# Kernel tuning notes

Hardware: AMD Instinct MI355X
Metric: run time of the kernel (lower is better)

The kernel has to match this reference:

```python
import jax, jax.numpy as jnp
import numpy as np

WIDTH = 36
N = WIDTH * WIDTH          # 1296 graph nodes per patch
SIGMA = 0.01               # weight_sigma
ZMAX = 0.01                # support_zmax
U_MIN, U_MAX = 0.001, 1.0
N_ITERS = 9                # 1 initial qpsolve + 8 glr refinements


def _build_graph():
    # 4-connected grid graph on WIDTH x WIDTH pixels -> incidence matrix H [E, N]
    nodes = np.arange(N).reshape(WIDTH, WIDTH)
    i0 = np.concatenate([nodes[:, :-1].ravel(), nodes[:-1, :].ravel()])
    i1 = np.concatenate([nodes[:, 1:].ravel(), nodes[1:, :].ravel()])
    E = i0.shape[0]  # 2520
    H = np.zeros((E, N), np.float32)
    H[np.arange(E), i0] = 1.0
    H[np.arange(E), i1] = -1.0
    return i0.astype(np.int32), i1.astype(np.int32), H


def setup_inputs() -> dict:
    key = jax.random.key(0)
    ks = jax.random.split(key, 6)
    B = 2
    i0, i1, H = _build_graph()
    std = 0.02  # weights_init_normal
    return {
        "xf": jax.random.normal(ks[0], (B, 3, WIDTH, WIDTH), jnp.float32),
        "u_param": jax.random.uniform(ks[1], (1,), jnp.float32),
        "H": jnp.asarray(H),
        "cw_in": std * jax.random.normal(ks[2], (32, 3, 3, 3), jnp.float32),
        "b_in": jnp.zeros((32,), jnp.float32),
        "cw_mid": std * jax.random.normal(ks[3], (5, 32, 32, 3, 3), jnp.float32),
        "b_mid": jnp.zeros((5, 32), jnp.float32),
        "cw_out": std * jax.random.normal(ks[4], (6, 32, 3, 3), jnp.float32),
        "b_out": jnp.zeros((6,), jnp.float32),
        "idx0": jnp.asarray(i0),
        "idx1": jnp.asarray(i1),
    }


def _conv(x, w, b):
    y = jax.lax.conv_general_dilated(x, w, (1, 1), "SAME",
                                     dimension_numbers=("NCHW", "OIHW", "NCHW"))
    return y + b[None, :, None, None]


def _cnnf(x, cw_in, b_in, cw_mid, b_mid, cw_out, b_out):
    h = jax.nn.relu(_conv(x, cw_in, b_in))
    for i in range(cw_mid.shape[0]):
        h = jax.nn.relu(_conv(h, cw_mid[i], b_mid[i]))
    return _conv(h, cw_out, b_out)


def _forward(xf, u_param, H, cw_in, b_in, cw_mid, b_mid, cw_out, b_out, idx0, idx1):
    B, C = xf.shape[0], xf.shape[1]
    Ne = idx0.shape[0]
    u = jnp.clip(u_param, U_MIN, U_MAX)[0]  # cnnu == uu(): scalar u, clamped

    y = xf.reshape(B, C, N, 1)
    # edge weights from deep features: w = exp(-sum_f (H f)^2 / sigma^2)
    feat = _cnnf(xf, cw_in, b_in, cw_mid, b_mid, cw_out, b_out).reshape(B, 6, N, 1)
    Fs = jnp.einsum("en,bfno->bfeo", H, feat) ** 2          # [B,6,E,1]
    w = jnp.exp(-Fs.sum(axis=1) / (SIGMA ** 2))              # [B,E,1]
    wv = jnp.broadcast_to(w[:, None, :, 0], (B, C, Ne))      # repeat over channels

    eye = jnp.eye(N, dtype=xf.dtype)
    base = jnp.zeros((B, C, N, N), xf.dtype)                 # base_W

    def step(y):
        z = jnp.einsum("en,bcno->bceo", H, y)                # per-edge diffs [B,C,E,1]
        za = jnp.abs(z[..., 0])                              # [B,C,E]
        Wm = base.at[:, :, idx0, idx1].set(wv).at[:, :, idx1, idx0].set(wv)
        Zm = base.at[:, :, idx0, idx1].set(za).at[:, :, idx1, idx0].set(za)
        Zm = jnp.maximum(Zm, ZMAX)
        Lm = Wm / Zm                                         # reweighted adjacency
        deg = Lm.sum(axis=-1)                                # L @ ones(N,1)
        L = deg[..., :, None] * eye - Lm                     # graph Laplacian
        # qpsolve: GLR closed form  (I + u L) x = y
        return jnp.linalg.solve(eye + u * L, y)

    for _ in range(N_ITERS):
        y = step(y)
    return y.reshape(B, C, WIDTH, WIDTH)


def reference(xf, u_param, H, cw_in, b_in, cw_mid, b_mid, cw_out, b_out, idx0, idx1):
    return _forward(xf, u_param, H, cw_in, b_in, cw_mid, b_mid, cw_out, b_out, idx0, idx1)
```

## Files before the change

### kernel.cpp

```cpp
#include <hip/hip_runtime.h>
#include <math.h>

#define NN 1296
#define OFF 40
#define TOT (OFF + NN + 40)
#define KMAX 240
#define PXW 21

__global__ __launch_bounds__(256) void conv_in_k(
    const float* __restrict__ in, const float* __restrict__ wgt,
    const float* __restrict__ bias, float* __restrict__ out)
{
  const int gid = blockIdx.x * 256 + threadIdx.x;
  const int wid = gid >> 6, lane = gid & 63;
  if (wid >= 2 * 32 * PXW) return;
  const int px = (wid % PXW) * 64 + lane;
  const int co = __builtin_amdgcn_readfirstlane((wid / PXW) % 32);
  const int b  = __builtin_amdgcn_readfirstlane(wid / (PXW * 32));
  if (px >= NN) return;

  const int py = px / 36, pxx = px % 36;
  int offs[9]; float msk[9];
#pragma unroll
  for (int dy = 0; dy < 3; ++dy)
#pragma unroll
    for (int dx = 0; dx < 3; ++dx) {
      const int yy = py + dy - 1, xx = pxx + dx - 1;
      const bool okp = ((unsigned)yy < 36u) && ((unsigned)xx < 36u);
      offs[dy * 3 + dx] = okp ? (yy * 36 + xx) : 0;
      msk[dy * 3 + dx]  = okp ? 1.f : 0.f;
    }

  float acc = bias[co];
  const float* __restrict__ inp = in + (size_t)b * 3 * NN;
  const float* __restrict__ wB  = wgt + (size_t)co * 3 * 9;
#pragma unroll
  for (int ci = 0; ci < 3; ++ci) {
    float v[9];
#pragma unroll
    for (int k9 = 0; k9 < 9; ++k9) v[k9] = msk[k9] * inp[ci * NN + offs[k9]];
#pragma unroll
    for (int k9 = 0; k9 < 9; ++k9) acc = fmaf(v[k9], wB[ci * 9 + k9], acc);
  }
  out[(size_t)(b * 32 + co) * NN + px] = fmaxf(acc, 0.f);
}

__global__ __launch_bounds__(256) void conv_mid2_k(
    const float* __restrict__ in, const float* __restrict__ wgt,
    const float* __restrict__ bias, float* __restrict__ out)
{
  const int blk = blockIdx.x;
  const int pxg = blk % PXW;
  const int cog = (blk / PXW) & 3;
  const int b   = blk / (PXW * 4);
  const int lane = threadIdx.x & 63;
  const int ciq  = __builtin_amdgcn_readfirstlane(threadIdx.x >> 6);
  const int px   = pxg * 64 + lane;
  const bool ok  = px < NN;

  __shared__ float part[4][8][64];

  float acc[8] = {0.f, 0.f, 0.f, 0.f, 0.f, 0.f, 0.f, 0.f};
  if (ok) {
    const int py = px / 36, pxx = px % 36;
    int offs[9]; float msk[9];
#pragma unroll
    for (int dy = 0; dy < 3; ++dy)
#pragma unroll
      for (int dx = 0; dx < 3; ++dx) {
        const int yy = py + dy - 1, xx = pxx + dx - 1;
        const bool okp = ((unsigned)yy < 36u) && ((unsigned)xx < 36u);
        offs[dy * 3 + dx] = okp ? (yy * 36 + xx) : 0;
        msk[dy * 3 + dx]  = okp ? 1.f : 0.f;
      }
    const float* __restrict__ inp = in + ((size_t)b * 32 + ciq * 8) * NN;
    const float* __restrict__ wB = wgt + ((size_t)(cog * 8) * 32 + ciq * 8) * 9;
#pragma unroll
    for (int ci = 0; ci < 8; ++ci) {
      float v[9];
#pragma unroll
      for (int k9 = 0; k9 < 9; ++k9) v[k9] = msk[k9] * inp[ci * NN + offs[k9]];
#pragma unroll
      for (int t = 0; t < 8; ++t)
#pragma unroll
        for (int k9 = 0; k9 < 9; ++k9)
          acc[t] = fmaf(v[k9], wB[(t * 32 + ci) * 9 + k9], acc[t]);
    }
  }
#pragma unroll
  for (int t = 0; t < 8; ++t) part[ciq][t][lane] = acc[t];
  __syncthreads();
  if (ok) {
#pragma unroll
    for (int tt = 0; tt < 2; ++tt) {
      const int t = ciq + tt * 4;
      float s = part[0][t][lane] + part[1][t][lane]
              + part[2][t][lane] + part[3][t][lane] + bias[cog * 8 + t];
      s = fmaxf(s, 0.f);
      out[((size_t)b * 32 + cog * 8 + t) * NN + px] = s;
    }
  }
}

template<int COUT, bool RELU>
__global__ __launch_bounds__(256) void conv_mid_k(
    const float* __restrict__ in, const float* __restrict__ wgt,
    const float* __restrict__ bias, float* __restrict__ out)
{
  const int blk = blockIdx.x;
  const int pxg = blk % PXW;
  const int co  = (blk / PXW) % COUT;
  const int b   = blk / (PXW * COUT);
  const int lane = threadIdx.x & 63;
  const int ciq  = threadIdx.x >> 6;
  const int px   = pxg * 64 + lane;
  const bool ok  = px < NN;

  __shared__ float part[4][64];

  float acc = 0.f;
  if (ok) {
    const int py = px / 36, pxx = px % 36;
    int offs[9]; float msk[9];
#pragma unroll
    for (int dy = 0; dy < 3; ++dy)
#pragma unroll
      for (int dx = 0; dx < 3; ++dx) {
        const int yy = py + dy - 1, xx = pxx + dx - 1;
        const bool okp = ((unsigned)yy < 36u) && ((unsigned)xx < 36u);
        offs[dy * 3 + dx] = okp ? (yy * 36 + xx) : 0;
        msk[dy * 3 + dx]  = okp ? 1.f : 0.f;
      }
    const float* __restrict__ inp = in + ((size_t)b * 32 + ciq * 8) * NN;
    const float* __restrict__ wB  = wgt + ((size_t)co * 32 + ciq * 8) * 9;
#pragma unroll
    for (int ci = 0; ci < 8; ++ci) {
      float v[9];
#pragma unroll
      for (int k9 = 0; k9 < 9; ++k9) v[k9] = msk[k9] * inp[ci * NN + offs[k9]];
#pragma unroll
      for (int k9 = 0; k9 < 9; ++k9) acc = fmaf(v[k9], wB[ci * 9 + k9], acc);
    }
  }
  part[ciq][lane] = acc;
  __syncthreads();
  if (threadIdx.x < 64 && ok) {
    float s = part[0][lane] + part[1][lane] + part[2][lane] + part[3][lane]
            + bias[co];
    if (RELU) s = fmaxf(s, 0.f);
    out[((size_t)b * COUT + co) * NN + px] = s;
  }
}

__global__ __launch_bounds__(384) void gtv_k(
    const float* __restrict__ xf, const float* __restrict__ up,
    const float* __restrict__ feat, float* __restrict__ out)
{
  const int sys = blockIdx.x, b = sys / 3, ch = sys % 3;
  const int tid = threadIdx.x;
  const int wave = tid >> 6, lane = tid & 63;
  const bool act = tid < 324;
  const int qq = act ? tid : 0;
  const int i0 = OFF + 4 * qq;

  __shared__ __align__(16) float ysL[TOT], ahL[TOT], avL[TOT], dA[TOT], dB[TOT];
  __shared__ float red[16];

  float u = up[0]; u = fminf(fmaxf(u, 0.001f), 1.0f);

  if (tid < OFF) {
    const int t2 = OFF + NN + tid;
    ysL[tid] = 0.f; ahL[tid] = 0.f; avL[tid] = 0.f; dA[tid] = 0.f; dB[tid] = 0.f;
    ysL[t2] = 0.f; ahL[t2] = 0.f; avL[t2] = 0.f; dA[t2] = 0.f; dB[t2] = 0.f;
  }

  const float* __restrict__ xfB = xf + (size_t)(b * 3 + ch) * NN;
  float wh4[4] = {0.f, 0.f, 0.f, 0.f}, wv4[4] = {0.f, 0.f, 0.f, 0.f};
  if (act) {
    *(float4*)&ysL[i0] = *(const float4*)&xfB[4 * qq];
#pragma unroll
    for (int j = 0; j < 4; ++j) {
      const int n = 4 * qq + j;
      const int col = n % 36, row = n / 36;
      float sh = 0.f, sv = 0.f;
#pragma unroll
      for (int f = 0; f < 6; ++f) {
        const float* __restrict__ fp = feat + (size_t)(b * 6 + f) * NN;
        const float a = fp[n];
        if (col < 35) { const float d = a - fp[n + 1];  sh += d * d; }
        if (row < 35) { const float d = a - fp[n + 36]; sv += d * d; }
      }
      wh4[j] = (col < 35) ? expf(-sh * 1e4f) : 0.f;
      wv4[j] = (row < 35) ? expf(-sv * 1e4f) : 0.f;
    }
  }
  __syncthreads();

  float x[4] = {0.f, 0.f, 0.f, 0.f};

  for (int it = 0; it < 9; ++it) {
    float4 yv = make_float4(0,0,0,0), yD = make_float4(0,0,0,0);
    float yR = 0.f;
    float ah[4] = {0,0,0,0}, av[4] = {0,0,0,0};
    if (act) {
      yv = *(const float4*)&ysL[i0];
      yR = ysL[i0 + 4];
      yD = *(const float4*)&ysL[i0 + 36];
      ah[0] = u * wh4[0] / fmaxf(fabsf(yv.x - yv.y), 0.01f);
      ah[1] = u * wh4[1] / fmaxf(fabsf(yv.y - yv.z), 0.01f);
      ah[2] = u * wh4[2] / fmaxf(fabsf(yv.z - yv.w), 0.01f);
      ah[3] = u * wh4[3] / fmaxf(fabsf(yv.w - yR  ), 0.01f);
      av[0] = u * wv4[0] / fmaxf(fabsf(yv.x - yD.x), 0.01f);
      av[1] = u * wv4[1] / fmaxf(fabsf(yv.y - yD.y), 0.01f);
      av[2] = u * wv4[2] / fmaxf(fabsf(yv.z - yD.z), 0.01f);
      av[3] = u * wv4[3] / fmaxf(fabsf(yv.w - yD.w), 0.01f);
      *(float4*)&ahL[i0] = make_float4(ah[0], ah[1], ah[2], ah[3]);
      *(float4*)&avL[i0] = make_float4(av[0], av[1], av[2], av[3]);
    }
    __syncthreads();

    float cL[4], cR[4], cU[4], cD[4], cc[4], bn[4], os[4];
    float mo = 0.f, me = 0.f;
    if (act) {
      const float cl0 = ahL[i0 - 1];
      const float4 aU = *(const float4*)&avL[i0 - 36];
      cL[0] = cl0;  cL[1] = ah[0]; cL[2] = ah[1]; cL[3] = ah[2];
      cR[0] = ah[0]; cR[1] = ah[1]; cR[2] = ah[2]; cR[3] = ah[3];
      cU[0] = aU.x; cU[1] = aU.y; cU[2] = aU.z; cU[3] = aU.w;
      cD[0] = av[0]; cD[1] = av[1]; cD[2] = av[2]; cD[3] = av[3];
      bn[0] = yv.x; bn[1] = yv.y; bn[2] = yv.z; bn[3] = yv.w;
#pragma unroll
      for (int j = 0; j < 4; ++j) {
        os[j] = cL[j] + cR[j] + cU[j] + cD[j];
        cc[j] = 1.f + os[j];
        mo = fmaxf(mo, os[j]);
      }
      const float ahR  = ahL[i0 + 4];
      const float avRu = avL[i0 - 32];
      const float avR  = avL[i0 + 4];
      const float osR  = ah[3] + ahR + avRu + avR;
      const float ahDl = ahL[i0 + 35];
      const float4 ahD = *(const float4*)&ahL[i0 + 36];
      const float4 avD = *(const float4*)&avL[i0 + 36];
      float osD[4];
      osD[0] = ahDl  + ahD.x + av[0] + avD.x;
      osD[1] = ahD.x + ahD.y + av[1] + avD.y;
      osD[2] = ahD.y + ahD.z + av[2] + avD.z;
      osD[3] = ahD.z + ahD.w + av[3] + avD.w;
      const float osN[4] = { os[1], os[2], os[3], osR };
#pragma unroll
      for (int j = 0; j < 4; ++j)
        me = fmaxf(me, os[j] + fmaxf(osN[j], osD[j]));
    } else {
#pragma unroll
      for (int j = 0; j < 4; ++j) {
        cL[j]=cR[j]=cU[j]=cD[j]=0.f; cc[j]=1.f; bn[j]=0.f; os[j]=0.f;
      }
    }
#pragma unroll
    for (int o = 32; o >= 1; o >>= 1) {
      mo = fmaxf(mo, __shfl_xor(mo, o));
      me = fmaxf(me, __shfl_xor(me, o));
    }
    if (lane == 0) { red[wave] = mo; red[8 + wave] = me; }
    __syncthreads();
    float m1 = fmaxf(fmaxf(red[0], red[1]),
               fmaxf(fmaxf(red[2], red[3]), fmaxf(red[4], red[5])));
    float m2 = fmaxf(fmaxf(red[8], red[9]),
               fmaxf(fmaxf(red[10], red[11]), fmaxf(red[12], red[13])));
    const float lmaxL = fminf(2.f * m1, m2);

    const float h     = 0.5f * lmaxL;
    const float theta = 1.f + h;
    const float del   = fmaxf(h, 1e-30f);
    const float sig1  = theta / del;
    const float rho0  = del / theta;
    const float kappa = 1.f + lmaxL;
    const float srk   = sqrtf(kappa);
    const float rc    = (srk - 1.f) / (srk + 1.f);

    float r[4], d[4];
    float rmx = 0.f;
    if (act) {
      const float bl = ysL[i0 - 1];
      const float4 bu = *(const float4*)&ysL[i0 - 36];
      const float uu[4] = {bu.x, bu.y, bu.z, bu.w};
      const float dd[4] = {yD.x, yD.y, yD.z, yD.w};
#pragma unroll
      for (int j = 0; j < 4; ++j) {
        const float nl = (j == 0) ? bl : bn[j - 1];
        const float nr = (j == 3) ? yR : bn[j + 1];
        const float Ab = cc[j] * bn[j] - cL[j] * nl - cR[j] * nr
                       - cU[j] * uu[j] - cD[j] * dd[j];
        x[j] = bn[j];
        r[j] = bn[j] - Ab;
        d[j] = r[j] / theta;
        rmx = fmaxf(rmx, fabsf(r[j]));
      }
      *(float4*)&dB[i0] = make_float4(d[0], d[1], d[2], d[3]);
    } else {
#pragma unroll
      for (int j = 0; j < 4; ++j) { r[j] = 0.f; d[j] = 0.f; x[j] = 0.f; }
    }
#pragma unroll
    for (int o = 32; o >= 1; o >>= 1) rmx = fmaxf(rmx, __shfl_xor(rmx, o));
    if (lane == 0) red[wave] = rmx;
    __syncthreads();
    const float rmax0 = fmaxf(fmaxf(red[0], red[1]),
                       fmaxf(fmaxf(red[2], red[3]), fmaxf(red[4], red[5])));

    int kcap;
    if (rmax0 <= 5e-4f) kcap = 0;
    else if (rc < 1e-10f) kcap = 1;
    else {
      kcap = (int)ceilf(8.0f / (-logf(rc)));
      kcap = (kcap < 1) ? 1 : (kcap > KMAX ? KMAX : kcap);
    }
    const float eps = fmaxf(rmax0 * 3.3e-4f, 2.5e-4f);

    float rho = rho0;
    float* dc = dB; float* dnx = dA;
    for (int k = 0; k < kcap; ++k) {
      if (k >= 4 && (k & 3) == 0) {
        const float rmc = fmaxf(fmaxf(red[0], red[1]),
                         fmaxf(fmaxf(red[2], red[3]), fmaxf(red[4], red[5])));
        if (rmc <= eps) break;
      }
      const float rn = 1.f / (2.f * sig1 - rho);
      const float cd = rn * rho, cr = 2.f * rn / del;
      rho = rn;
      if (act) {
        const float dl = dc[i0 - 1], dr = dc[i0 + 4];
        const float4 u4 = *(const float4*)&dc[i0 - 36];
        const float4 d4 = *(const float4*)&dc[i0 + 36];
        const float uu[4] = {u4.x, u4.y, u4.z, u4.w};
        const float dd[4] = {d4.x, d4.y, d4.z, d4.w};
        float dn[4];
#pragma unroll
        for (int j = 0; j < 4; ++j) {
          const float nl = (j == 0) ? dl : d[j - 1];
          const float nr = (j == 3) ? dr : d[j + 1];
          const float Ad = cc[j] * d[j] - cL[j] * nl - cR[j] * nr
                         - cU[j] * uu[j] - cD[j] * dd[j];
          x[j] += d[j];
          r[j] -= Ad;
          dn[j] = cd * d[j] + cr * r[j];
        }
        *(float4*)&dnx[i0] = make_float4(dn[0], dn[1], dn[2], dn[3]);
#pragma unroll
        for (int j = 0; j < 4; ++j) d[j] = dn[j];
      }
      if ((k & 3) == 3) {
        float rm = 0.f;
        if (act) {
          rm = fmaxf(fmaxf(fabsf(r[0]), fabsf(r[1])),
                     fmaxf(fabsf(r[2]), fabsf(r[3])));
        }
#pragma unroll
        for (int o = 32; o >= 1; o >>= 1) rm = fmaxf(rm, __shfl_xor(rm, o));
        if (lane == 0) red[wave] = rm;
      }
      __syncthreads();
      float* t = dc; dc = dnx; dnx = t;
    }

    if (act) *(float4*)&ysL[i0] = make_float4(x[0], x[1], x[2], x[3]);
    __syncthreads();
  }

  if (act) *(float4*)&out[(size_t)(b * 3 + ch) * NN + 4 * qq]
      = make_float4(x[0], x[1], x[2], x[3]);
}

extern "C" void kernel_launch(void* const* d_in, const int* in_sizes, int n_in,
                              void* d_out, int out_size, void* d_ws, size_t ws_size,
                              hipStream_t stream) {
  const float* xf     = (const float*)d_in[0];
  const float* up     = (const float*)d_in[1];
  const float* cw_in  = (const float*)d_in[3];
  const float* b_in   = (const float*)d_in[4];
  const float* cw_mid = (const float*)d_in[5];
  const float* b_mid  = (const float*)d_in[6];
  const float* cw_out = (const float*)d_in[7];
  const float* b_out  = (const float*)d_in[8];

  float* ws   = (float*)d_ws;
  float* hb0  = ws;
  float* hb1  = hb0 + 82944;
  float* feat = hb1 + 82944;

  conv_in_k<<<dim3(336), dim3(256), 0, stream>>>(xf, cw_in, b_in, hb0);
  const float* src = hb0; float* dst = hb1;
  for (int i = 0; i < 5; ++i) {
    conv_mid2_k<<<dim3(2 * 4 * PXW), dim3(256), 0, stream>>>(
        src, cw_mid + i * 9216, b_mid + i * 32, dst);
    const float* t = dst; dst = (float*)src; src = t;
  }
  conv_mid_k<6, false><<<dim3(2 * 6 * PXW), dim3(256), 0, stream>>>(
      src, cw_out, b_out, feat);

  gtv_k<<<dim3(6), dim3(384), 0, stream>>>(xf, up, feat, (float*)d_out);
}
```

Measured before the change: 121.9 us.

## Fuse output conv into GTV solver and drop early-exit residual checks

The final 32->6 convolution is folded into the GTV solver kernel, so each block computes the feature maps into shared memory rather than launching a separate kernel and going through global memory. The periodic residual max-reduction and early-break test inside the Chebyshev-style iteration loop are removed, and the iteration-count heuristic constant drops from 8 to 7. This removes one launch and the per-4-iteration reduction overhead. In exchange, only 6 blocks now compute the output conv redundantly (each recomputes all 6 features per batch), and the loop always runs its full capped count, which may cost accuracy or extra iterations.

```diff
diff --git a/kernel.cpp b/kernel.cpp
--- a/kernel.cpp
+++ b/kernel.cpp
@@ -102,59 +102,10 @@
   }
 }
 
-template<int COUT, bool RELU>
-__global__ __launch_bounds__(256) void conv_mid_k(
-    const float* __restrict__ in, const float* __restrict__ wgt,
-    const float* __restrict__ bias, float* __restrict__ out)
-{
-  const int blk = blockIdx.x;
-  const int pxg = blk % PXW;
-  const int co  = (blk / PXW) % COUT;
-  const int b   = blk / (PXW * COUT);
-  const int lane = threadIdx.x & 63;
-  const int ciq  = threadIdx.x >> 6;
-  const int px   = pxg * 64 + lane;
-  const bool ok  = px < NN;
-
-  __shared__ float part[4][64];
-
-  float acc = 0.f;
-  if (ok) {
-    const int py = px / 36, pxx = px % 36;
-    int offs[9]; float msk[9];
-#pragma unroll
-    for (int dy = 0; dy < 3; ++dy)
-#pragma unroll
-      for (int dx = 0; dx < 3; ++dx) {
-        const int yy = py + dy - 1, xx = pxx + dx - 1;
-        const bool okp = ((unsigned)yy < 36u) && ((unsigned)xx < 36u);
-        offs[dy * 3 + dx] = okp ? (yy * 36 + xx) : 0;
-        msk[dy * 3 + dx]  = okp ? 1.f : 0.f;
-      }
-    const float* __restrict__ inp = in + ((size_t)b * 32 + ciq * 8) * NN;
-    const float* __restrict__ wB  = wgt + ((size_t)co * 32 + ciq * 8) * 9;
-#pragma unroll
-    for (int ci = 0; ci < 8; ++ci) {
-      float v[9];
-#pragma unroll
-      for (int k9 = 0; k9 < 9; ++k9) v[k9] = msk[k9] * inp[ci * NN + offs[k9]];
-#pragma unroll
-      for (int k9 = 0; k9 < 9; ++k9) acc = fmaf(v[k9], wB[ci * 9 + k9], acc);
-    }
-  }
-  part[ciq][lane] = acc;
-  __syncthreads();
-  if (threadIdx.x < 64 && ok) {
-    float s = part[0][lane] + part[1][lane] + part[2][lane] + part[3][lane]
-            + bias[co];
-    if (RELU) s = fmaxf(s, 0.f);
-    out[((size_t)b * COUT + co) * NN + px] = s;
-  }
-}
-
 __global__ __launch_bounds__(384) void gtv_k(
     const float* __restrict__ xf, const float* __restrict__ up,
-    const float* __restrict__ feat, float* __restrict__ out)
+    const float* __restrict__ mid, const float* __restrict__ cw_out,
+    const float* __restrict__ b_out, float* __restrict__ out)
 {
   const int sys = blockIdx.x, b = sys / 3, ch = sys % 3;
   const int tid = threadIdx.x;
@@ -164,6 +115,7 @@
   const int i0 = OFF + 4 * qq;
 
   __shared__ __align__(16) float ysL[TOT], ahL[TOT], avL[TOT], dA[TOT], dB[TOT];
+  __shared__ float featL[6 * NN];
   __shared__ float red[16];
 
   float u = up[0]; u = fminf(fmaxf(u, 0.001f), 1.0f);
@@ -175,9 +127,45 @@
   }
 
   const float* __restrict__ xfB = xf + (size_t)(b * 3 + ch) * NN;
+  if (act) {
+    *(float4*)&ysL[i0] = *(const float4*)&xfB[4 * qq];
+    const float* __restrict__ mB = mid + (size_t)b * 32 * NN;
+#pragma unroll
+    for (int j = 0; j < 4; ++j) {
+      const int n = 4 * qq + j;
+      const int py = n / 36, pxx = n % 36;
+      int offs[9]; float msk[9];
+#pragma unroll
+      for (int dy = 0; dy < 3; ++dy)
+#pragma unroll
+        for (int dx = 0; dx < 3; ++dx) {
+          const int yy = py + dy - 1, xx = pxx + dx - 1;
+          const bool okp = ((unsigned)yy < 36u) && ((unsigned)xx < 36u);
+          offs[dy * 3 + dx] = okp ? (yy * 36 + xx) : 0;
+          msk[dy * 3 + dx]  = okp ? 1.f : 0.f;
+        }
+      float accf[6];
+#pragma unroll
+      for (int f = 0; f < 6; ++f) accf[f] = b_out[f];
+#pragma unroll
+      for (int ci = 0; ci < 32; ++ci) {
+        float v[9];
+#pragma unroll
+        for (int k9 = 0; k9 < 9; ++k9) v[k9] = msk[k9] * mB[ci * NN + offs[k9]];
+#pragma unroll
+        for (int f = 0; f < 6; ++f)
+#pragma unroll
+          for (int k9 = 0; k9 < 9; ++k9)
+            accf[f] = fmaf(v[k9], cw_out[(f * 32 + ci) * 9 + k9], accf[f]);
+      }
+#pragma unroll
+      for (int f = 0; f < 6; ++f) featL[f * NN + n] = accf[f];
+    }
+  }
+  __syncthreads();
+
   float wh4[4] = {0.f, 0.f, 0.f, 0.f}, wv4[4] = {0.f, 0.f, 0.f, 0.f};
   if (act) {
-    *(float4*)&ysL[i0] = *(const float4*)&xfB[4 * qq];
 #pragma unroll
     for (int j = 0; j < 4; ++j) {
       const int n = 4 * qq + j;
@@ -185,7 +173,7 @@
       float sh = 0.f, sv = 0.f;
 #pragma unroll
       for (int f = 0; f < 6; ++f) {
-        const float* __restrict__ fp = feat + (size_t)(b * 6 + f) * NN;
+        const float* __restrict__ fp = featL + f * NN;
         const float a = fp[n];
         if (col < 35) { const float d = a - fp[n + 1];  sh += d * d; }
         if (row < 35) { const float d = a - fp[n + 36]; sv += d * d; }
@@ -313,19 +301,13 @@
     if (rmax0 <= 5e-4f) kcap = 0;
     else if (rc < 1e-10f) kcap = 1;
     else {
-      kcap = (int)ceilf(8.0f / (-logf(rc)));
+      kcap = (int)ceilf(7.0f / (-logf(rc)));
       kcap = (kcap < 1) ? 1 : (kcap > KMAX ? KMAX : kcap);
     }
-    const float eps = fmaxf(rmax0 * 3.3e-4f, 2.5e-4f);
 
     float rho = rho0;
     float* dc = dB; float* dnx = dA;
     for (int k = 0; k < kcap; ++k) {
-      if (k >= 4 && (k & 3) == 0) {
-        const float rmc = fmaxf(fmaxf(red[0], red[1]),
-                         fmaxf(fmaxf(red[2], red[3]), fmaxf(red[4], red[5])));
-        if (rmc <= eps) break;
-      }
       const float rn = 1.f / (2.f * sig1 - rho);
       const float cd = rn * rho, cr = 2.f * rn / del;
       rho = rn;
@@ -349,16 +331,6 @@
         *(float4*)&dnx[i0] = make_float4(dn[0], dn[1], dn[2], dn[3]);
 #pragma unroll
         for (int j = 0; j < 4; ++j) d[j] = dn[j];
-      }
-      if ((k & 3) == 3) {
-        float rm = 0.f;
-        if (act) {
-          rm = fmaxf(fmaxf(fabsf(r[0]), fabsf(r[1])),
-                     fmaxf(fabsf(r[2]), fabsf(r[3])));
-        }
-#pragma unroll
-        for (int o = 32; o >= 1; o >>= 1) rm = fmaxf(rm, __shfl_xor(rm, o));
-        if (lane == 0) red[wave] = rm;
       }
       __syncthreads();
       float* t = dc; dc = dnx; dnx = t;
@@ -384,10 +356,9 @@
   const float* cw_out = (const float*)d_in[7];
   const float* b_out  = (const float*)d_in[8];
 
-  float* ws   = (float*)d_ws;
-  float* hb0  = ws;
-  float* hb1  = hb0 + 82944;
-  float* feat = hb1 + 82944;
+  float* ws  = (float*)d_ws;
+  float* hb0 = ws;
+  float* hb1 = hb0 + 82944;
 
   conv_in_k<<<dim3(336), dim3(256), 0, stream>>>(xf, cw_in, b_in, hb0);
   const float* src = hb0; float* dst = hb1;
@@ -396,8 +367,7 @@
         src, cw_mid + i * 9216, b_mid + i * 32, dst);
     const float* t = dst; dst = (float*)src; src = t;
   }
-  conv_mid_k<6, false><<<dim3(2 * 6 * PXW), dim3(256), 0, stream>>>(
-      src, cw_out, b_out, feat);
-
-  gtv_k<<<dim3(6), dim3(384), 0, stream>>>(xf, up, feat, (float*)d_out);
+
+  gtv_k<<<dim3(6), dim3(384), 0, stream>>>(xf, up, src, cw_out, b_out,
+                                           (float*)d_out);
 }
```

Measured after the change: 271.2 us. +122.4%, slower.
